# Performance work log

Measured on AMD Instinct MI355X. Metric: run time of the kernel, lower is better.

Reference implementation:

```python
import jax, jax.numpy as jnp
import numpy as np

RADIUS = 2.0      # ball radius (meters)
NSAMPLE = 32      # max neighbors per ball
B = 4             # number of scenes (batch)
NPB = 4096        # points per scene (equal counts assumed)
C = 20            # number of semantic classes
CUBE = 20.0       # points live in a [0,20]^3 m cube


def setup_inputs() -> dict:
    key = jax.random.key(0)
    k1, k2, k3 = jax.random.split(key, 3)
    xyz = jax.random.uniform(k1, (B * NPB, 3), jnp.float32) * CUBE
    pred = jax.random.normal(k2, (B * NPB, C), jnp.float32)
    labels = jax.random.randint(k3, (B * NPB,), 0, C)
    tgt = jax.nn.one_hot(labels, C, dtype=jnp.float32)
    cnt = jnp.full((B,), NPB, dtype=jnp.int32)
    # module asserts new_xyz == xyz and equal batch counts
    return {"xyz": xyz, "xyz_batch_cnt": cnt, "pred": pred, "tgt": tgt,
            "new_xyz": xyz, "new_xyz_batch_cnt": cnt}


def _ball_query(xyz_b, new_xyz_b, radius, nsample):
    """xyz_b, new_xyz_b: (B, n, 3). Returns local idx (B, n, nsample).
    Replicates pointnet2 stack ball_query: first `nsample` points (in index
    order) with squared distance < radius^2; unfilled slots repeat the first
    found index. Indices are local to each batch segment."""
    n = xyz_b.shape[1]
    d2 = jnp.sum((new_xyz_b[:, :, None, :] - xyz_b[:, None, :, :]) ** 2, axis=-1)  # (B,n,n)
    mask = d2 < radius * radius
    # score = point index if inside ball else sentinel n; smallest scores = first hits
    score = jnp.where(mask, jnp.arange(n, dtype=jnp.int32), jnp.int32(n))
    neg_vals, _ = jax.lax.top_k(-score, nsample)   # largest of -score == smallest score
    idx = -neg_vals                                # (B,n,nsample), ascending index order
    first = idx[:, :, :1]                          # first found index (self is always in-ball)
    idx = jnp.where(idx == n, first, idx)          # fill empty slots with first index
    return idx


def _group(feats_b, idx_b):
    """feats_b: (B, n, C); idx_b: (B, m, nsample) local indices -> (B, m, nsample, C)."""
    b = jnp.arange(feats_b.shape[0])[:, None, None]
    return feats_b[b, idx_b]


def reference(xyz, xyz_batch_cnt, pred, tgt, new_xyz, new_xyz_batch_cnt):
    nb = xyz_batch_cnt.shape[0]
    n = xyz.shape[0] // nb                 # equal per-batch counts
    xyz_b = xyz.reshape(nb, n, 3)
    new_xyz_b = new_xyz.reshape(nb, n, 3)

    idx_b = _ball_query(xyz_b, new_xyz_b, RADIUS, NSAMPLE)   # (B,n,ns)
    m = nb * n
    idx = idx_b.reshape(m, NSAMPLE)

    # grouping_operation -> (M, C, nsample)
    grouped_pred = _group(pred.reshape(nb, n, -1), idx_b).reshape(m, NSAMPLE, -1).transpose(0, 2, 1)
    grouped_tgt = _group(tgt.reshape(nb, n, -1), idx_b).reshape(m, NSAMPLE, -1).transpose(0, 2, 1)

    # since new_xyz == xyz, every ball contains its own center -> empty_ball_mask
    # is all-False and the nonempty filtering in the torch code is the identity.
    pred_local_relation = grouped_pred - pred[:, :, None]
    tgt_local_relation = grouped_tgt - tgt[:, :, None]

    # weight (computed under no_grad in torch)
    eq = idx == idx[:, :1]
    not_eq = ~eq
    not_eq = not_eq.at[:, 0].set(True)
    a = not_eq.astype(jnp.float32)
    weight = a / jnp.sum(a, axis=-1, keepdims=True)
    return (pred_local_relation, tgt_local_relation, weight)
```

## Files before the change

### kernel.cpp

```cpp
#include <hip/hip_runtime.h>

#define NS 32
#define GD 10
#define NCXY (GD * GD)
#define COLCAP 128
#define WCAP 64
#define INV_CELL 0.5f
#define MARGIN 1e-3f

static __device__ __forceinline__ int lane_rank(unsigned long long m) {
    return __builtin_amdgcn_mbcnt_hi((unsigned)(m >> 32),
                                     __builtin_amdgcn_mbcnt_lo((unsigned)m, 0u));
}

static __device__ __forceinline__ void wave_lds_fence() {
    __builtin_amdgcn_fence(__ATOMIC_ACQ_REL, "wavefront");
    __builtin_amdgcn_wave_barrier();
}

__global__ __launch_bounds__(256) void build_kernel(
    const float* __restrict__ xyz, int n,
    int* __restrict__ colOff, float4* __restrict__ pts)
{
    __shared__ float4 hl[4][WCAP];
    __shared__ int    swcnt[4];
    __shared__ float4 merged[COLCAP];

    const int col  = blockIdx.x;
    const int b    = col / NCXY;
    const int cxy  = col - b * NCXY;
    const int mycx = cxy / GD;
    const int mycy = cxy - mycx * GD;
    const int lane = threadIdx.x & 63;
    const int wv   = threadIdx.x >> 6;
    const float* __restrict__ px = xyz + (size_t)b * n * 3;

    const int per = (n + 3) >> 2;
    const int j0  = wv * per;
    const int j1  = min(j0 + per, n);
    int cnt = 0;
    for (int it = j0; it < j1; it += 64) {
        const int  j   = it + lane;
        const bool inb = j < j1;
        const int  jc  = inb ? j : 0;
        const float x = px[3 * jc], y = px[3 * jc + 1], z = px[3 * jc + 2];
        const int cx = min(max((int)floorf(x * INV_CELL), 0), GD - 1);
        const int cy = min(max((int)floorf(y * INV_CELL), 0), GD - 1);
        const bool hit = inb && (cx == mycx) && (cy == mycy);
        const unsigned long long m = __ballot(hit);
        if (m) {
            const int zc  = min(max((int)floorf(z * INV_CELL), 0), GD - 1);
            const int pos = cnt + lane_rank(m);
            if (hit && pos < WCAP)
                hl[wv][pos] = make_float4(x, y, z, __int_as_float((zc << 12) | j));
            cnt += __popcll(m);
        }
    }
    if (lane == 0) swcnt[wv] = cnt < WCAP ? cnt : WCAP;
    __syncthreads();

    const int p0 = swcnt[0], p1 = p0 + swcnt[1], p2 = p1 + swcnt[2], p3 = p2 + swcnt[3];
    const int h  = p3 < COLCAP ? p3 : COLCAP;
    if (wv == 0) {
        for (int g = lane; g < h; g += 64) {
            const int w   = (g >= p0) + (g >= p1) + (g >= p2);
            const int off = g - (w == 0 ? 0 : (w == 1 ? p0 : (w == 2 ? p1 : p2)));
            merged[g] = hl[w][off];
        }
    }
    __syncthreads();

    if (wv == 0) {
        int czc[GD];
        #pragma unroll
        for (int k = 0; k < GD; ++k) czc[k] = 0;
        for (int r = 0; r < h; r += 64) {
            const int t = r + lane;
            int zc = -1;
            if (t < h) zc = __float_as_int(merged[t].w) >> 12;
            #pragma unroll
            for (int k = 0; k < GD; ++k)
                czc[k] += __popcll(__ballot(zc == k));
        }
        int off[GD + 1];
        off[0] = 0;
        #pragma unroll
        for (int k = 0; k < GD; ++k) off[k + 1] = off[k] + czc[k];

        int cur[GD];
        #pragma unroll
        for (int k = 0; k < GD; ++k) cur[k] = off[k];

        for (int r = 0; r < h; r += 64) {
            const int t = r + lane;
            int zc = -1, pl = 0;
            float4 f = make_float4(0.f, 0.f, 0.f, 0.f);
            if (t < h) { f = merged[t]; pl = __float_as_int(f.w); zc = pl >> 12; }
            #pragma unroll
            for (int k = 0; k < GD; ++k) {
                const unsigned long long mk = __ballot(zc == k);
                if (zc == k) {
                    const int pos = cur[k] + lane_rank(mk);
                    pts[(size_t)col * COLCAP + pos] =
                        make_float4(f.x, f.y, f.z, __int_as_float(pl & 4095));
                }
                cur[k] += __popcll(mk);
            }
        }
        if (lane == 0) {
            const int bo = col * 11;
            #pragma unroll
            for (int k = 0; k < GD; ++k) colOff[bo + k] = off[k];
            colOff[bo + GD] = h;
        }
    }
}

template <int C>
__global__ __launch_bounds__(256) void query2_kernel(
    const float* __restrict__ new_xyz,
    const float* __restrict__ pred, const float* __restrict__ tgt,
    const int* __restrict__ colOff, const float4* __restrict__ pts,
    int n, int total,
    float* __restrict__ out0, float* __restrict__ out1, float* __restrict__ wout)
{
#pragma clang fp contract(off)
    __shared__ int spref[4][2][17];
    __shared__ int sgb[4][2][16];
    __shared__ int slist[4][2][64];
    __shared__ int sorted[4][2][32];

    const int lane = threadIdx.x & 63;
    const int wv   = __builtin_amdgcn_readfirstlane(threadIdx.x >> 6);
    int q0w = blockIdx.x * 8 + wv * 2;
    if (q0w > total - 2) q0w = total - 2;
    const int b    = q0w / n;
    const int base = b * n;

    const float qx0 = new_xyz[q0w * 3 + 0], qy0 = new_xyz[q0w * 3 + 1], qz0 = new_xyz[q0w * 3 + 2];
    const float qx1 = new_xyz[q0w * 3 + 3], qy1 = new_xyz[q0w * 3 + 4], qz1 = new_xyz[q0w * 3 + 5];

    int cx0a = max((int)floorf((qx0 - 2.0f - MARGIN) * INV_CELL), 0);
    int cx1a = min((int)floorf((qx0 + 2.0f + MARGIN) * INV_CELL), GD - 1);
    int cy0a = max((int)floorf((qy0 - 2.0f - MARGIN) * INV_CELL), 0);
    int cy1a = min((int)floorf((qy0 + 2.0f + MARGIN) * INV_CELL), GD - 1);
    int cz0a = max((int)floorf((qz0 - 2.0f - MARGIN) * INV_CELL), 0);
    int cz1a = min((int)floorf((qz0 + 2.0f + MARGIN) * INV_CELL), GD - 1);
    const int nya = cy1a - cy0a + 1;
    const int nr0 = __builtin_amdgcn_readfirstlane((cx1a - cx0a + 1) * nya);

    int cx0b = max((int)floorf((qx1 - 2.0f - MARGIN) * INV_CELL), 0);
    int cx1b = min((int)floorf((qx1 + 2.0f + MARGIN) * INV_CELL), GD - 1);
    int cy0b = max((int)floorf((qy1 - 2.0f - MARGIN) * INV_CELL), 0);
    int cy1b = min((int)floorf((qy1 + 2.0f + MARGIN) * INV_CELL), GD - 1);
    int cz0b = max((int)floorf((qz1 - 2.0f - MARGIN) * INV_CELL), 0);
    int cz1b = min((int)floorf((qz1 + 2.0f + MARGIN) * INV_CELL), GD - 1);
    const int nyb = cy1b - cy0b + 1;
    const int nr1 = __builtin_amdgcn_readfirstlane((cx1b - cx0b + 1) * nyb);

    int cc = 0, gb = 0;
    if (lane < nr0) {
        const int rx   = lane / nya;
        const int ry   = lane - rx * nya;
        const int ccol = b * NCXY + (cx0a + rx) * GD + (cy0a + ry);
        const int o0   = colOff[ccol * 11 + cz0a];
        const int o1   = colOff[ccol * 11 + cz1a + 1];
        gb = ccol * COLCAP + o0;
        cc = o1 - o0;
    } else if (lane >= 32 && lane < 32 + nr1) {
        const int r    = lane - 32;
        const int rx   = r / nyb;
        const int ry   = r - rx * nyb;
        const int ccol = b * NCXY + (cx0b + rx) * GD + (cy0b + ry);
        const int o0   = colOff[ccol * 11 + cz0b];
        const int o1   = colOff[ccol * 11 + cz1b + 1];
        gb = ccol * COLCAP + o0;
        cc = o1 - o0;
    }
    int run = cc;
    #pragma unroll
    for (int off = 1; off < 32; off <<= 1) {
        int y = __shfl_up(run, off, 64);
        if ((lane & 31) >= off) run += y;
    }
    const int T0 = __shfl(run, nr0 - 1, 64);
    const int T1 = __shfl(run, 32 + nr1 - 1, 64);

    if (lane < 16) spref[wv][0][lane + 1] = run;
    else if (lane >= 32 && lane < 48) spref[wv][1][lane - 31] = run;
    if (lane == 0) { spref[wv][0][0] = 0; spref[wv][1][0] = 0; }
    if (lane < nr0) sgb[wv][0][lane] = gb;
    else if (lane >= 32 && lane < 32 + nr1) sgb[wv][1][lane - 32] = gb;

    wave_lds_fence();

    const int maxT = T0 > T1 ? T0 : T1;
    int tot0 = 0, tot1 = 0;
    for (int r = 0; r < maxT; r += 64) {
        const int  t    = r + lane;
        const bool actA = t < T0;
        const bool actB = t < T1;
        const int  tca  = actA ? t : 0;
        const int  tcb  = actB ? t : 0;
        int kA = 0, kB = 0;
        #pragma unroll
        for (int step = 8; step >= 1; step >>= 1) {
            if (spref[wv][0][kA + step] <= tca) kA += step;
            if (spref[wv][1][kB + step] <= tcb) kB += step;
        }
        const int aiA = sgb[wv][0][kA] + (tca - spref[wv][0][kA]);
        const int aiB = sgb[wv][1][kB] + (tcb - spref[wv][1][kB]);
        const float4 fA = pts[aiA];
        const float4 fB = pts[aiB];

        float dxA = qx0 - fA.x, dyA = qy0 - fA.y, dzA = qz0 - fA.z;
        const float d2A = (dxA * dxA + dyA * dyA) + dzA * dzA;
        float dxB = qx1 - fB.x, dyB = qy1 - fB.y, dzB = qz1 - fB.z;
        const float d2B = (dxB * dxB + dyB * dyB) + dzB * dzB;
        const bool hitA = actA && (d2A < 4.0f);
        const bool hitB = actB && (d2B < 4.0f);

        const unsigned long long mA = __ballot(hitA);
        const int posA = tot0 + lane_rank(mA);
        if (hitA && posA < 64) slist[wv][0][posA] = __float_as_int(fA.w);
        tot0 += __popcll(mA);
        const unsigned long long mB = __ballot(hitB);
        const int posB = tot1 + lane_rank(mB);
        if (hitB && posB < 64) slist[wv][1][posB] = __float_as_int(fB.w);
        tot1 += __popcll(mB);
    }

    wave_lds_fence();

    const int qs = lane >> 5;
    const int s  = lane & 31;
    if (tot0 <= 32 && tot1 <= 32) {
        const int totq = qs ? tot1 : tot0;
        int v = (s < totq) ? slist[wv][qs][s] : 0x7fffffff;
        #pragma unroll
        for (int k = 2; k <= 32; k <<= 1) {
            #pragma unroll
            for (int j = k >> 1; j >= 1; j >>= 1) {
                const int  o     = __shfl_xor(v, j, 32);
                const bool up    = ((s & k) == 0);
                const bool lower = ((s & j) == 0);
                const int  mn = v < o ? v : o;
                const int  mx = v < o ? o : v;
                v = (lower == up) ? mn : mx;
            }
        }
        sorted[wv][qs][s] = v;
    } else {
        #pragma unroll 1
        for (int qq = 0; qq < 2; ++qq) {
            const int totq = qq ? tot1 : tot0;
            const int totv = totq < 64 ? totq : 64;
            int v = (lane < totv) ? slist[wv][qq][lane] : 0x7fffffff;
            #pragma unroll
            for (int k = 2; k <= 64; k <<= 1) {
                #pragma unroll
                for (int j = k >> 1; j >= 1; j >>= 1) {
                    const int  o     = __shfl_xor(v, j, 64);
                    const bool up    = ((lane & k) == 0);
                    const bool lower = ((lane & j) == 0);
                    const int  mn = v < o ? v : o;
                    const int  mx = v < o ? o : v;
                    v = (lower == up) ? mn : mx;
                }
            }
            if (lane < 32) sorted[wv][qq][lane] = v;
        }
    }

    wave_lds_fence();

    const int tc0 = tot0 < NS ? tot0 : NS;
    const int tc1 = tot1 < NS ? tot1 : NS;
    {
        const int tcq = qs ? tc1 : tc0;
        const int tcm = tcq > 0 ? tcq : 1;
        wout[(size_t)q0w * NS + lane] = (s < tcm) ? 1.0f / (float)tcm : 0.0f;
    }

    const float* __restrict__ src = qs ? tgt : pred;
    float* __restrict__ dst       = qs ? out1 : out0;
    #pragma unroll
    for (int qq = 0; qq < 2; ++qq) {
        const int qg    = q0w + qq;
        const int totq  = qq ? tot1 : tot0;
        const int tcq   = qq ? tc1 : tc0;
        const int first = (totq > 0) ? sorted[wv][qq][0] : (n - 1);
        const int jl    = (s < tcq) ? sorted[wv][qq][s] : first;

        const float4* __restrict__ nb = (const float4*)(src + (size_t)(base + jl) * C);
        const float4* __restrict__ ct = (const float4*)(src + (size_t)qg * C);
        float* __restrict__ o = dst + (size_t)qg * (C * NS) + s;
        #pragma unroll
        for (int c4 = 0; c4 < C / 4; ++c4) {
            const float4 a = nb[c4], bq = ct[c4];
            o[(c4 * 4 + 0) * NS] = a.x - bq.x;
            o[(c4 * 4 + 1) * NS] = a.y - bq.y;
            o[(c4 * 4 + 2) * NS] = a.z - bq.z;
            o[(c4 * 4 + 3) * NS] = a.w - bq.w;
        }
        #pragma unroll
        for (int c = (C / 4) * 4; c < C; ++c)
            o[c * NS] = src[(size_t)(base + jl) * C + c] - src[(size_t)qg * C + c];
    }
}

template <int C>
__global__ __launch_bounds__(256) void fused_brute_kernel(
    const float* __restrict__ xyz, const float* __restrict__ new_xyz,
    const float* __restrict__ pred, const float* __restrict__ tgt,
    int n, int total, float* __restrict__ out0, float* __restrict__ out1,
    float* __restrict__ wout)
{
#pragma clang fp contract(off)
    __shared__ int sidx[8][NS];

    const int lane = threadIdx.x & 63;
    const int wv   = __builtin_amdgcn_readfirstlane(threadIdx.x >> 6);
    int q0 = (blockIdx.x * 4 + wv) * 2;
    if (q0 > total - 2) q0 = total - 2;
    const int base = (q0 / n) * n;

    const float ax0 = new_xyz[q0 * 3 + 0], ay0 = new_xyz[q0 * 3 + 1], az0 = new_xyz[q0 * 3 + 2];
    const float ax1 = new_xyz[q0 * 3 + 3], ay1 = new_xyz[q0 * 3 + 4], az1 = new_xyz[q0 * 3 + 5];
    const float* __restrict__ px = xyz + (size_t)base * 3;

    int tot0 = 0, tot1 = 0, first0 = n - 1, first1 = n - 1;
    for (int it = 0; it < n; it += 64) {
        const int ja  = it + lane;
        const int jca = ja < n ? ja : n - 1;
        const float xa = px[jca * 3 + 0], ya = px[jca * 3 + 1], za = px[jca * 3 + 2];
        float dx = ax0 - xa, dy = ay0 - ya, dz = az0 - za;
        const float d0 = (dx * dx + dy * dy) + dz * dz;
        dx = ax1 - xa; dy = ay1 - ya; dz = az1 - za;
        const float d1 = (dx * dx + dy * dy) + dz * dz;
        const bool h0 = (ja < n) & (d0 < 4.0f);
        const bool h1 = (ja < n) & (d1 < 4.0f);
        const unsigned long long m0 = __ballot(h0);
        if (m0) {
            if (tot0 == 0) first0 = it + __builtin_ctzll(m0);
            const int pos = tot0 + lane_rank(m0);
            if (h0 && pos < NS) sidx[wv * 2 + 0][pos] = ja;
            tot0 += __popcll(m0);
        }
        const unsigned long long m1 = __ballot(h1);
        if (m1) {
            if (tot1 == 0) first1 = it + __builtin_ctzll(m1);
            const int pos = tot1 + lane_rank(m1);
            if (h1 && pos < NS) sidx[wv * 2 + 1][pos] = ja;
            tot1 += __popcll(m1);
        }
    }

    const int s  = lane & 31;
    const int qs = lane >> 5;
    {
        const int tt    = qs ? tot1 : tot0;
        const int first = qs ? first1 : first0;
        const int tc    = tt < NS ? tt : NS;
        if (s >= tc) sidx[wv * 2 + qs][s] = first;
        const int tcm = tc > 0 ? tc : 1;
        wout[(size_t)q0 * NS + lane] = (s < tcm) ? 1.0f / (float)tcm : 0.0f;
    }
    __syncthreads();

    const int q  = q0 + qs;
    const int jl = sidx[wv * 2 + qs][s];
    const float4* __restrict__ nb_p = (const float4*)(pred + (size_t)(base + jl) * C);
    const float4* __restrict__ nb_t = (const float4*)(tgt  + (size_t)(base + jl) * C);
    const float4* __restrict__ ct_p = (const float4*)(pred + (size_t)q * C);
    const float4* __restrict__ ct_t = (const float4*)(tgt  + (size_t)q * C);
    float* __restrict__ o0 = out0 + (size_t)q * (C * NS) + s;
    float* __restrict__ o1 = out1 + (size_t)q * (C * NS) + s;
    #pragma unroll
    for (int c4 = 0; c4 < C / 4; ++c4) {
        const float4 a = nb_p[c4], bq = ct_p[c4];
        o0[(c4 * 4 + 0) * NS] = a.x - bq.x;
        o0[(c4 * 4 + 1) * NS] = a.y - bq.y;
        o0[(c4 * 4 + 2) * NS] = a.z - bq.z;
        o0[(c4 * 4 + 3) * NS] = a.w - bq.w;
        const float4 u = nb_t[c4], vv = ct_t[c4];
        o1[(c4 * 4 + 0) * NS] = u.x - vv.x;
        o1[(c4 * 4 + 1) * NS] = u.y - vv.y;
        o1[(c4 * 4 + 2) * NS] = u.z - vv.z;
        o1[(c4 * 4 + 3) * NS] = u.w - vv.w;
    }
}

extern "C" void kernel_launch(void* const* d_in, const int* in_sizes, int n_in,
                              void* d_out, int out_size, void* d_ws, size_t ws_size,
                              hipStream_t stream)
{
    const float* xyz     = (const float*)d_in[0];
    const float* pred    = (const float*)d_in[2];
    const float* tgt     = (const float*)d_in[3];
    const float* new_xyz = (const float*)d_in[4];

    const int total = in_sizes[0] / 3;
    const int nb    = in_sizes[1];
    const int n     = total / nb;
    const int C     = in_sizes[2] / total;

    float* out = (float*)d_out;
    const size_t relsz = (size_t)total * C * NS;
    float* out0 = out;
    float* out1 = out + relsz;
    float* wout = out + 2 * relsz;

    const int ncols = nb * NCXY;
    const size_t ws_need = (size_t)ncols * COLCAP * sizeof(float4)
                         + (size_t)ncols * 11 * sizeof(int);

    if (C == 20 && (n % 8) == 0 && ws_size >= ws_need) {
        float4* pts    = (float4*)d_ws;
        int*    colOff = (int*)((char*)d_ws + (size_t)ncols * COLCAP * sizeof(float4));

        build_kernel<<<ncols, 256, 0, stream>>>(xyz, n, colOff, pts);
        query2_kernel<20><<<(total + 7) / 8, 256, 0, stream>>>(
            new_xyz, pred, tgt, colOff, pts, n, total, out0, out1, wout);
    } else if (C == 20) {
        fused_brute_kernel<20><<<(total + 7) / 8, 256, 0, stream>>>(
            xyz, new_xyz, pred, tgt, n, total, out0, out1, wout);
    }
    (void)n_in; (void)out_size;
}
```

Measured before the change: 35.41 us.

## Bin queries by grid column and stage 3x3 neighbor points in LDS

Queries are now binned into the same x-y grid columns as the source points. Each block takes a slice of one query column and first stages all points of the 3x3 neighboring columns into shared memory, so every query in that column reuses them instead of gathering candidates from global memory per query. The build kernel runs twice as many blocks so it bins both point sets in one launch. In exchange every query now scans the full 3x3 column stack without z-range pruning, staging is capped at 768 points, and queries are written in spatially sorted order, which scatters the output writes.

Result: slower. 39.36 us (+11.1%).

```diff
diff --git a/kernel.cpp b/kernel.cpp
--- a/kernel.cpp
+++ b/kernel.cpp
@@ -5,8 +5,8 @@
 #define NCXY (GD * GD)
 #define COLCAP 128
 #define WCAP 64
+#define SCAP 768
 #define INV_CELL 0.5f
-#define MARGIN 1e-3f
 
 static __device__ __forceinline__ int lane_rank(unsigned long long m) {
     return __builtin_amdgcn_mbcnt_hi((unsigned)(m >> 32),
@@ -19,21 +19,28 @@
 }
 
 __global__ __launch_bounds__(256) void build_kernel(
-    const float* __restrict__ xyz, int n,
-    int* __restrict__ colOff, float4* __restrict__ pts)
+    const float* __restrict__ xyz, const float* __restrict__ qxyz,
+    int n, int ncols,
+    int* __restrict__ colOff, float4* __restrict__ pts,
+    int* __restrict__ qcolOff, float4* __restrict__ qpts)
 {
     __shared__ float4 hl[4][WCAP];
     __shared__ int    swcnt[4];
     __shared__ float4 merged[COLCAP];
 
-    const int col  = blockIdx.x;
+    const int bk = blockIdx.x;
+    const float* __restrict__ srcp = (bk < ncols) ? xyz : qxyz;
+    int*        __restrict__ co    = (bk < ncols) ? colOff : qcolOff;
+    float4*     __restrict__ po    = (bk < ncols) ? pts : qpts;
+    const int col  = (bk < ncols) ? bk : bk - ncols;
+
     const int b    = col / NCXY;
     const int cxy  = col - b * NCXY;
     const int mycx = cxy / GD;
     const int mycy = cxy - mycx * GD;
     const int lane = threadIdx.x & 63;
     const int wv   = threadIdx.x >> 6;
-    const float* __restrict__ px = xyz + (size_t)b * n * 3;
+    const float* __restrict__ px = srcp + (size_t)b * n * 3;
 
     const int per = (n + 3) >> 2;
     const int j0  = wv * per;
@@ -101,7 +108,7 @@
                 const unsigned long long mk = __ballot(zc == k);
                 if (zc == k) {
                     const int pos = cur[k] + lane_rank(mk);
-                    pts[(size_t)col * COLCAP + pos] =
+                    po[(size_t)col * COLCAP + pos] =
                         make_float4(f.x, f.y, f.z, __int_as_float(pl & 4095));
                 }
                 cur[k] += __popcll(mk);
@@ -110,202 +117,187 @@
         if (lane == 0) {
             const int bo = col * 11;
             #pragma unroll
-            for (int k = 0; k < GD; ++k) colOff[bo + k] = off[k];
-            colOff[bo + GD] = h;
+            for (int k = 0; k < GD; ++k) co[bo + k] = off[k];
+            co[bo + GD] = h;
         }
     }
 }
 
 template <int C>
-__global__ __launch_bounds__(256) void query2_kernel(
-    const float* __restrict__ new_xyz,
+__global__ __launch_bounds__(256) void query_staged_kernel(
     const float* __restrict__ pred, const float* __restrict__ tgt,
     const int* __restrict__ colOff, const float4* __restrict__ pts,
-    int n, int total,
-    float* __restrict__ out0, float* __restrict__ out1, float* __restrict__ wout)
+    const int* __restrict__ qcolOff, const float4* __restrict__ qpts,
+    int n, float* __restrict__ out0, float* __restrict__ out1,
+    float* __restrict__ wout)
 {
 #pragma clang fp contract(off)
-    __shared__ int spref[4][2][17];
-    __shared__ int sgb[4][2][16];
-    __shared__ int slist[4][2][64];
-    __shared__ int sorted[4][2][32];
-
-    const int lane = threadIdx.x & 63;
-    const int wv   = __builtin_amdgcn_readfirstlane(threadIdx.x >> 6);
-    int q0w = blockIdx.x * 8 + wv * 2;
-    if (q0w > total - 2) q0w = total - 2;
-    const int b    = q0w / n;
-    const int base = b * n;
-
-    const float qx0 = new_xyz[q0w * 3 + 0], qy0 = new_xyz[q0w * 3 + 1], qz0 = new_xyz[q0w * 3 + 2];
-    const float qx1 = new_xyz[q0w * 3 + 3], qy1 = new_xyz[q0w * 3 + 4], qz1 = new_xyz[q0w * 3 + 5];
-
-    int cx0a = max((int)floorf((qx0 - 2.0f - MARGIN) * INV_CELL), 0);
-    int cx1a = min((int)floorf((qx0 + 2.0f + MARGIN) * INV_CELL), GD - 1);
-    int cy0a = max((int)floorf((qy0 - 2.0f - MARGIN) * INV_CELL), 0);
-    int cy1a = min((int)floorf((qy0 + 2.0f + MARGIN) * INV_CELL), GD - 1);
-    int cz0a = max((int)floorf((qz0 - 2.0f - MARGIN) * INV_CELL), 0);
-    int cz1a = min((int)floorf((qz0 + 2.0f + MARGIN) * INV_CELL), GD - 1);
-    const int nya = cy1a - cy0a + 1;
-    const int nr0 = __builtin_amdgcn_readfirstlane((cx1a - cx0a + 1) * nya);
-
-    int cx0b = max((int)floorf((qx1 - 2.0f - MARGIN) * INV_CELL), 0);
-    int cx1b = min((int)floorf((qx1 + 2.0f + MARGIN) * INV_CELL), GD - 1);
-    int cy0b = max((int)floorf((qy1 - 2.0f - MARGIN) * INV_CELL), 0);
-    int cy1b = min((int)floorf((qy1 + 2.0f + MARGIN) * INV_CELL), GD - 1);
-    int cz0b = max((int)floorf((qz1 - 2.0f - MARGIN) * INV_CELL), 0);
-    int cz1b = min((int)floorf((qz1 + 2.0f + MARGIN) * INV_CELL), GD - 1);
-    const int nyb = cy1b - cy0b + 1;
-    const int nr1 = __builtin_amdgcn_readfirstlane((cx1b - cx0b + 1) * nyb);
-
-    int cc = 0, gb = 0;
-    if (lane < nr0) {
-        const int rx   = lane / nya;
-        const int ry   = lane - rx * nya;
-        const int ccol = b * NCXY + (cx0a + rx) * GD + (cy0a + ry);
-        const int o0   = colOff[ccol * 11 + cz0a];
-        const int o1   = colOff[ccol * 11 + cz1a + 1];
-        gb = ccol * COLCAP + o0;
-        cc = o1 - o0;
-    } else if (lane >= 32 && lane < 32 + nr1) {
-        const int r    = lane - 32;
-        const int rx   = r / nyb;
-        const int ry   = r - rx * nyb;
-        const int ccol = b * NCXY + (cx0b + rx) * GD + (cy0b + ry);
-        const int o0   = colOff[ccol * 11 + cz0b];
-        const int o1   = colOff[ccol * 11 + cz1b + 1];
-        gb = ccol * COLCAP + o0;
-        cc = o1 - o0;
-    }
-    int run = cc;
-    #pragma unroll
-    for (int off = 1; off < 32; off <<= 1) {
-        int y = __shfl_up(run, off, 64);
-        if ((lane & 31) >= off) run += y;
-    }
-    const int T0 = __shfl(run, nr0 - 1, 64);
-    const int T1 = __shfl(run, 32 + nr1 - 1, 64);
-
-    if (lane < 16) spref[wv][0][lane + 1] = run;
-    else if (lane >= 32 && lane < 48) spref[wv][1][lane - 31] = run;
-    if (lane == 0) { spref[wv][0][0] = 0; spref[wv][1][0] = 0; }
-    if (lane < nr0) sgb[wv][0][lane] = gb;
-    else if (lane >= 32 && lane < 32 + nr1) sgb[wv][1][lane - 32] = gb;
-
-    wave_lds_fence();
-
-    const int maxT = T0 > T1 ? T0 : T1;
-    int tot0 = 0, tot1 = 0;
-    for (int r = 0; r < maxT; r += 64) {
-        const int  t    = r + lane;
-        const bool actA = t < T0;
-        const bool actB = t < T1;
-        const int  tca  = actA ? t : 0;
-        const int  tcb  = actB ? t : 0;
-        int kA = 0, kB = 0;
+    __shared__ float4 lpts[SCAP];
+    __shared__ int    spre[10];
+    __shared__ int    sgb9[9];
+    __shared__ int    slist[4][2][64];
+    __shared__ int    sorted[4][2][32];
+
+    const int tid   = threadIdx.x, lane = tid & 63, wv = tid >> 6;
+    const int blk   = blockIdx.x;
+    const int col   = blk >> 3;
+    const int slice = blk & 7;
+    const int b     = col / NCXY;
+    const int cxy   = col - b * NCXY;
+    const int ccx   = cxy / GD, ccy = cxy - ccx * GD;
+    const int base  = b * n;
+
+    const int qh = qcolOff[col * 11 + GD];
+    if (qh == 0) return;
+
+    if (wv == 0) {
+        int cnt = 0, gbase = 0;
+        if (lane < 9) {
+            const int dxo = lane / 3 - 1, dyo = lane % 3 - 1;
+            const int nx = ccx + dxo, ny2 = ccy + dyo;
+            if (nx >= 0 && nx < GD && ny2 >= 0 && ny2 < GD) {
+                const int nc = b * NCXY + nx * GD + ny2;
+                cnt   = colOff[nc * 11 + GD];
+                gbase = nc * COLCAP;
+            }
+        }
+        int run = cnt;
+        #pragma unroll
+        for (int off = 1; off < 16; off <<= 1) {
+            int y = __shfl_up(run, off, 64);
+            if (lane >= off) run += y;
+        }
+        if (lane < 9) { spre[lane + 1] = run; sgb9[lane] = gbase; }
+        if (lane == 0) spre[0] = 0;
+    }
+    __syncthreads();
+
+    int T9 = spre[9];
+    if (T9 > SCAP) T9 = SCAP;
+
+    for (int g = tid; g < T9; g += 256) {
+        int k = 0;
         #pragma unroll
         for (int step = 8; step >= 1; step >>= 1) {
-            if (spref[wv][0][kA + step] <= tca) kA += step;
-            if (spref[wv][1][kB + step] <= tcb) kB += step;
-        }
-        const int aiA = sgb[wv][0][kA] + (tca - spref[wv][0][kA]);
-        const int aiB = sgb[wv][1][kB] + (tcb - spref[wv][1][kB]);
-        const float4 fA = pts[aiA];
-        const float4 fB = pts[aiB];
-
-        float dxA = qx0 - fA.x, dyA = qy0 - fA.y, dzA = qz0 - fA.z;
-        const float d2A = (dxA * dxA + dyA * dyA) + dzA * dzA;
-        float dxB = qx1 - fB.x, dyB = qy1 - fB.y, dzB = qz1 - fB.z;
-        const float d2B = (dxB * dxB + dyB * dyB) + dzB * dzB;
-        const bool hitA = actA && (d2A < 4.0f);
-        const bool hitB = actB && (d2B < 4.0f);
-
-        const unsigned long long mA = __ballot(hitA);
-        const int posA = tot0 + lane_rank(mA);
-        if (hitA && posA < 64) slist[wv][0][posA] = __float_as_int(fA.w);
-        tot0 += __popcll(mA);
-        const unsigned long long mB = __ballot(hitB);
-        const int posB = tot1 + lane_rank(mB);
-        if (hitB && posB < 64) slist[wv][1][posB] = __float_as_int(fB.w);
-        tot1 += __popcll(mB);
-    }
-
-    wave_lds_fence();
-
-    const int qs = lane >> 5;
-    const int s  = lane & 31;
-    if (tot0 <= 32 && tot1 <= 32) {
-        const int totq = qs ? tot1 : tot0;
-        int v = (s < totq) ? slist[wv][qs][s] : 0x7fffffff;
-        #pragma unroll
-        for (int k = 2; k <= 32; k <<= 1) {
-            #pragma unroll
-            for (int j = k >> 1; j >= 1; j >>= 1) {
-                const int  o     = __shfl_xor(v, j, 32);
-                const bool up    = ((s & k) == 0);
-                const bool lower = ((s & j) == 0);
-                const int  mn = v < o ? v : o;
-                const int  mx = v < o ? o : v;
-                v = (lower == up) ? mn : mx;
-            }
-        }
-        sorted[wv][qs][s] = v;
-    } else {
-        #pragma unroll 1
-        for (int qq = 0; qq < 2; ++qq) {
-            const int totq = qq ? tot1 : tot0;
-            const int totv = totq < 64 ? totq : 64;
-            int v = (lane < totv) ? slist[wv][qq][lane] : 0x7fffffff;
-            #pragma unroll
-            for (int k = 2; k <= 64; k <<= 1) {
+            const int nk = k + step;
+            if (nk <= 8 && spre[nk] <= g) k = nk;
+        }
+        lpts[g] = pts[(size_t)sgb9[k] + (g - spre[k])];
+    }
+    __syncthreads();
+
+    const int qps = (qh + 7) >> 3;
+    const int j0  = slice * qps;
+    const int j1  = min(j0 + qps, qh);
+    const int qs  = lane >> 5, s = lane & 31;
+
+    for (int j = j0 + 2 * wv; j < j1; j += 8) {
+        const int jb  = (j + 1 < j1) ? j + 1 : j;
+        const float4 fq0 = qpts[(size_t)col * COLCAP + j];
+        const float4 fq1 = qpts[(size_t)col * COLCAP + jb];
+        const int q0g = base + __float_as_int(fq0.w);
+        const int q1g = base + __float_as_int(fq1.w);
+
+        int tot0 = 0, tot1 = 0;
+        for (int r = 0; r < T9; r += 64) {
+            const int  t   = r + lane;
+            const bool act = t < T9;
+            const float4 f = lpts[act ? t : 0];
+            float dxA = fq0.x - f.x, dyA = fq0.y - f.y, dzA = fq0.z - f.z;
+            const float d2A = (dxA * dxA + dyA * dyA) + dzA * dzA;
+            float dxB = fq1.x - f.x, dyB = fq1.y - f.y, dzB = fq1.z - f.z;
+            const float d2B = (dxB * dxB + dyB * dyB) + dzB * dzB;
+            const bool hitA = act && (d2A < 4.0f);
+            const bool hitB = act && (d2B < 4.0f);
+
+            const unsigned long long mA = __ballot(hitA);
+            const int posA = tot0 + lane_rank(mA);
+            if (hitA && posA < 64) slist[wv][0][posA] = __float_as_int(f.w);
+            tot0 += __popcll(mA);
+            const unsigned long long mB = __ballot(hitB);
+            const int posB = tot1 + lane_rank(mB);
+            if (hitB && posB < 64) slist[wv][1][posB] = __float_as_int(f.w);
+            tot1 += __popcll(mB);
+        }
+
+        wave_lds_fence();
+
+        if (tot0 <= 32 && tot1 <= 32) {
+            const int totq = qs ? tot1 : tot0;
+            int v = (s < totq) ? slist[wv][qs][s] : 0x7fffffff;
+            #pragma unroll
+            for (int k = 2; k <= 32; k <<= 1) {
                 #pragma unroll
-                for (int j = k >> 1; j >= 1; j >>= 1) {
-                    const int  o     = __shfl_xor(v, j, 64);
-                    const bool up    = ((lane & k) == 0);
-                    const bool lower = ((lane & j) == 0);
+                for (int jj = k >> 1; jj >= 1; jj >>= 1) {
+                    const int  o     = __shfl_xor(v, jj, 32);
+                    const bool up    = ((s & k) == 0);
+                    const bool lower = ((s & jj) == 0);
                     const int  mn = v < o ? v : o;
                     const int  mx = v < o ? o : v;
                     v = (lower == up) ? mn : mx;
                 }
             }
-            if (lane < 32) sorted[wv][qq][lane] = v;
-        }
-    }
-
-    wave_lds_fence();
-
-    const int tc0 = tot0 < NS ? tot0 : NS;
-    const int tc1 = tot1 < NS ? tot1 : NS;
-    {
-        const int tcq = qs ? tc1 : tc0;
-        const int tcm = tcq > 0 ? tcq : 1;
-        wout[(size_t)q0w * NS + lane] = (s < tcm) ? 1.0f / (float)tcm : 0.0f;
-    }
-
-    const float* __restrict__ src = qs ? tgt : pred;
-    float* __restrict__ dst       = qs ? out1 : out0;
-    #pragma unroll
-    for (int qq = 0; qq < 2; ++qq) {
-        const int qg    = q0w + qq;
-        const int totq  = qq ? tot1 : tot0;
-        const int tcq   = qq ? tc1 : tc0;
-        const int first = (totq > 0) ? sorted[wv][qq][0] : (n - 1);
-        const int jl    = (s < tcq) ? sorted[wv][qq][s] : first;
-
-        const float4* __restrict__ nb = (const float4*)(src + (size_t)(base + jl) * C);
-        const float4* __restrict__ ct = (const float4*)(src + (size_t)qg * C);
-        float* __restrict__ o = dst + (size_t)qg * (C * NS) + s;
-        #pragma unroll
-        for (int c4 = 0; c4 < C / 4; ++c4) {
-            const float4 a = nb[c4], bq = ct[c4];
-            o[(c4 * 4 + 0) * NS] = a.x - bq.x;
-            o[(c4 * 4 + 1) * NS] = a.y - bq.y;
-            o[(c4 * 4 + 2) * NS] = a.z - bq.z;
-            o[(c4 * 4 + 3) * NS] = a.w - bq.w;
-        }
-        #pragma unroll
-        for (int c = (C / 4) * 4; c < C; ++c)
-            o[c * NS] = src[(size_t)(base + jl) * C + c] - src[(size_t)qg * C + c];
+            sorted[wv][qs][s] = v;
+        } else {
+            #pragma unroll 1
+            for (int qq = 0; qq < 2; ++qq) {
+                const int totq = qq ? tot1 : tot0;
+                const int totv = totq < 64 ? totq : 64;
+                int v = (lane < totv) ? slist[wv][qq][lane] : 0x7fffffff;
+                #pragma unroll
+                for (int k = 2; k <= 64; k <<= 1) {
+                    #pragma unroll
+                    for (int jj = k >> 1; jj >= 1; jj >>= 1) {
+                        const int  o     = __shfl_xor(v, jj, 64);
+                        const bool up    = ((lane & k) == 0);
+                        const bool lower = ((lane & jj) == 0);
+                        const int  mn = v < o ? v : o;
+                        const int  mx = v < o ? o : v;
+                        v = (lower == up) ? mn : mx;
+                    }
+                }
+                if (lane < 32) sorted[wv][qq][lane] = v;
+            }
+        }
+
+        wave_lds_fence();
+
+        const int tc0 = tot0 < NS ? tot0 : NS;
+        const int tc1 = tot1 < NS ? tot1 : NS;
+        {
+            const int qg  = qs ? q1g : q0g;
+            const int tcq = qs ? tc1 : tc0;
+            const int tcm = tcq > 0 ? tcq : 1;
+            wout[(size_t)qg * NS + s] = (s < tcm) ? 1.0f / (float)tcm : 0.0f;
+        }
+
+        const float* __restrict__ src = qs ? tgt : pred;
+        float* __restrict__ dst       = qs ? out1 : out0;
+        #pragma unroll
+        for (int qq = 0; qq < 2; ++qq) {
+            const int qg    = qq ? q1g : q0g;
+            const int totq  = qq ? tot1 : tot0;
+            const int tcq   = qq ? tc1 : tc0;
+            const int first = (totq > 0) ? sorted[wv][qq][0] : (n - 1);
+            const int jl    = (s < tcq) ? sorted[wv][qq][s] : first;
+
+            const float4* __restrict__ nb = (const float4*)(src + (size_t)(base + jl) * C);
+            const float4* __restrict__ ct = (const float4*)(src + (size_t)qg * C);
+            float* __restrict__ o = dst + (size_t)qg * (C * NS) + s;
+            #pragma unroll
+            for (int c4 = 0; c4 < C / 4; ++c4) {
+                const float4 a = nb[c4], bq = ct[c4];
+                o[(c4 * 4 + 0) * NS] = a.x - bq.x;
+                o[(c4 * 4 + 1) * NS] = a.y - bq.y;
+                o[(c4 * 4 + 2) * NS] = a.z - bq.z;
+                o[(c4 * 4 + 3) * NS] = a.w - bq.w;
+            }
+            #pragma unroll
+            for (int c = (C / 4) * 4; c < C; ++c)
+                o[c * NS] = src[(size_t)(base + jl) * C + c] - src[(size_t)qg * C + c];
+        }
+
+        wave_lds_fence();
     }
 }
 
@@ -412,16 +404,20 @@
     float* wout = out + 2 * relsz;
 
     const int ncols = nb * NCXY;
-    const size_t ws_need = (size_t)ncols * COLCAP * sizeof(float4)
-                         + (size_t)ncols * 11 * sizeof(int);
-
-    if (C == 20 && (n % 8) == 0 && ws_size >= ws_need) {
-        float4* pts    = (float4*)d_ws;
-        int*    colOff = (int*)((char*)d_ws + (size_t)ncols * COLCAP * sizeof(float4));
-
-        build_kernel<<<ncols, 256, 0, stream>>>(xyz, n, colOff, pts);
-        query2_kernel<20><<<(total + 7) / 8, 256, 0, stream>>>(
-            new_xyz, pred, tgt, colOff, pts, n, total, out0, out1, wout);
+    const size_t ptsz  = (size_t)ncols * COLCAP * sizeof(float4);
+    const size_t offsz = (size_t)ncols * 11 * sizeof(int);
+    const size_t ws_need = 2 * ptsz + 2 * offsz;
+
+    if (C == 20 && ws_size >= ws_need) {
+        float4* pts     = (float4*)d_ws;
+        float4* qpts    = (float4*)((char*)d_ws + ptsz);
+        int*    colOff  = (int*)((char*)d_ws + 2 * ptsz);
+        int*    qcolOff = (int*)((char*)d_ws + 2 * ptsz + offsz);
+
+        build_kernel<<<2 * ncols, 256, 0, stream>>>(
+            xyz, new_xyz, n, ncols, colOff, pts, qcolOff, qpts);
+        query_staged_kernel<20><<<ncols * 8, 256, 0, stream>>>(
+            pred, tgt, colOff, pts, qcolOff, qpts, n, out0, out1, wout);
     } else if (C == 20) {
         fused_brute_kernel<20><<<(total + 7) / 8, 256, 0, stream>>>(
             xyz, new_xyz, pred, tgt, n, total, out0, out1, wout);
```
